# Performance work log

Hardware: AMD Instinct MI355X
Metric: run time of the kernel (lower is better)

The kernel has to match this reference:

```python
import jax, jax.numpy as jnp
import numpy as np

B, L, D = 2, 2048, 1024
H, DH = 16, 64
HIDDEN = 4096
DILATION, WINDOW, CAUSAL = 2, 512, True
EPS = 1e-5


def _ln(x, g, b):
    m = jnp.mean(x, axis=-1, keepdims=True)
    v = jnp.mean(jnp.square(x - m), axis=-1, keepdims=True)
    return (x - m) * jax.lax.rsqrt(v + EPS) * g + b


def setup_inputs() -> dict:
    key = jax.random.key(0)
    ks = jax.random.split(key, 8)
    s = 0.02
    return {
        "x": jax.random.normal(ks[0], (B, L, D), jnp.float32),
        "ln1_g": jnp.ones((D,), jnp.float32),
        "ln1_b": jnp.zeros((D,), jnp.float32),
        "w_qkv": jax.random.normal(ks[1], (3 * D, D), jnp.float32) * s,
        "b_qkv": jnp.zeros((3 * D,), jnp.float32),
        "w_o": jax.random.normal(ks[2], (D, D), jnp.float32) * s,
        "b_o": jnp.zeros((D,), jnp.float32),
        "ln2_g": jnp.ones((D,), jnp.float32),
        "ln2_b": jnp.zeros((D,), jnp.float32),
        "w_ff1": jax.random.normal(ks[3], (HIDDEN, D), jnp.float32) * s,
        "b_ff1": jnp.zeros((HIDDEN,), jnp.float32),
        "w_ff2": jax.random.normal(ks[4], (D, HIDDEN), jnp.float32) * s,
        "b_ff2": jnp.zeros((D,), jnp.float32),
    }


def reference(x, ln1_g, ln1_b, w_qkv, b_qkv, w_o, b_o, ln2_g, ln2_b, w_ff1, b_ff1, w_ff2, b_ff2):
    # pre-norm attention block with dilated/windowed/causal mask
    h = _ln(x, ln1_g, ln1_b)
    qkv = h @ w_qkv.T + b_qkv                      # [B, L, 3D]
    q, k, v = jnp.split(qkv, 3, axis=-1)
    q = q.reshape(B, L, H, DH)
    k = k.reshape(B, L, H, DH)
    v = v.reshape(B, L, H, DH)

    scale = 1.0 / jnp.sqrt(jnp.float32(DH))
    scores = jnp.einsum("bqhd,bkhd->bhqk", q, k) * scale  # [B, H, L, L]

    i = jnp.arange(L)[:, None]
    j = jnp.arange(L)[None, :]
    allowed = ((i - j) % DILATION == 0) & (jnp.abs(i - j) <= WINDOW)
    if CAUSAL:
        allowed = allowed & (j <= i)
    scores = jnp.where(allowed, scores, -jnp.inf)  # diagonal always allowed -> rows finite

    p = jax.nn.softmax(scores, axis=-1)
    attn = jnp.einsum("bhqk,bkhd->bqhd", p, v).reshape(B, L, D)

    out = x + attn @ w_o.T + b_o                   # residual 1 (dropout p=0)

    h2 = _ln(out, ln2_g, ln2_b)
    ff = jax.nn.gelu(h2 @ w_ff1.T + b_ff1, approximate=False) @ w_ff2.T + b_ff2
    return out + ff                                # residual 2
```

## Files before the change

kernel.cpp:

```cpp
#include <hip/hip_runtime.h>
#include <hip/hip_bf16.h>
#include <cmath>

#define Bsz 2
#define Lseq 2048
#define Dmod 1024
#define Hhead 16
#define DH 64
#define HID 4096
#define ROWS (Bsz * Lseq)
#define TD (3 * Dmod)

typedef __attribute__((ext_vector_type(8))) short bf16x8;
typedef __attribute__((ext_vector_type(4))) float f32x4;
typedef unsigned short ushort_t;

typedef const __attribute__((address_space(1))) void gv_t;
typedef __attribute__((address_space(3))) void lv_t;
#define GLDS16(GP, LP) __builtin_amdgcn_global_load_lds((gv_t*)(GP), (lv_t*)(LP), 16, 0, 0)

__device__ __forceinline__ float bf2f(short u)
{
    return __uint_as_float(((unsigned)(unsigned short)u) << 16);
}
__device__ __forceinline__ unsigned pack2(float a, float b)
{
    __hip_bfloat162 t;
    t.x = __float2bfloat16(a);
    t.y = __float2bfloat16(b);
    return *reinterpret_cast<unsigned*>(&t);
}
__device__ __forceinline__ float gelu_exact(float t)
{
    return 0.5f * t * (1.0f + erff(t * 0.70710678118654752f));
}

__device__ __forceinline__ void xcd_remap(int& mblk, int& nblk)
{
    int nx = gridDim.x;
    int nwg = nx * gridDim.y;
    int id = blockIdx.y * nx + blockIdx.x;
    int cpx = nwg >> 3;
    int swz = (id & 7) * cpx + (id >> 3);
    mblk = swz / nx;
    nblk = swz % nx;
}

__global__ __launch_bounds__(256) void f2b4_kernel(const float* __restrict__ s0, ushort_t* __restrict__ d0,
                                                   const float* __restrict__ s1, ushort_t* __restrict__ d1,
                                                   const float* __restrict__ s2, ushort_t* __restrict__ d2,
                                                   const float* __restrict__ s3, ushort_t* __restrict__ d3)
{
    int blk = blockIdx.x;
    const float* src;
    ushort_t* dst;
    int base;
    if (blk < 3072)      { src = s0; dst = d0; base = blk; }
    else if (blk < 4096) { src = s1; dst = d1; base = blk - 3072; }
    else if (blk < 8192) { src = s2; dst = d2; base = blk - 4096; }
    else                 { src = s3; dst = d3; base = blk - 8192; }
    int i = base * 256 + threadIdx.x;
    float4 v = reinterpret_cast<const float4*>(src)[i];
    uint2 o;
    o.x = pack2(v.x, v.y);
    o.y = pack2(v.z, v.w);
    reinterpret_cast<uint2*>(dst)[i] = o;
}

__global__ __launch_bounds__(256) void ln_kernel(const float* __restrict__ x,
                                                 const float* __restrict__ g,
                                                 const float* __restrict__ bta,
                                                 ushort_t* __restrict__ out)
{
    int row = blockIdx.x;
    int t = threadIdx.x;
    const float4* xr = reinterpret_cast<const float4*>(x) + (size_t)row * 256;
    float4 v = xr[t];
    float s  = v.x + v.y + v.z + v.w;
    float s2 = v.x * v.x + v.y * v.y + v.z * v.z + v.w * v.w;
#pragma unroll
    for (int o = 32; o > 0; o >>= 1) {
        s  += __shfl_down(s, o);
        s2 += __shfl_down(s2, o);
    }
    __shared__ float sa[4], sb[4];
    int wv = t >> 6, ln = t & 63;
    if (ln == 0) { sa[wv] = s; sb[wv] = s2; }
    __syncthreads();
    s  = sa[0] + sa[1] + sa[2] + sa[3];
    s2 = sb[0] + sb[1] + sb[2] + sb[3];
    float mean = s * (1.0f / 1024.0f);
    float var  = s2 * (1.0f / 1024.0f) - mean * mean;
    float inv  = rsqrtf(var + 1e-5f);
    float4 gv = reinterpret_cast<const float4*>(g)[t];
    float4 bv = reinterpret_cast<const float4*>(bta)[t];
    uint2 o;
    o.x = pack2((v.x - mean) * inv * gv.x + bv.x, (v.y - mean) * inv * gv.y + bv.y);
    o.y = pack2((v.z - mean) * inv * gv.z + bv.z, (v.w - mean) * inv * gv.w + bv.w);
    reinterpret_cast<uint2*>(out)[(size_t)row * 256 + t] = o;
}

__device__ __forceinline__ void gemm_n64_body(const ushort_t* __restrict__ A,
                                              const ushort_t* __restrict__ W,
                                              const float* __restrict__ bias,
                                              const float* __restrict__ res,
                                              void* __restrict__ C,
                                              int M, int N, int K, int ldw,
                                              int act, int obf)
{
    __shared__ ushort_t As0[128 * 64];
    __shared__ ushort_t Bs0[64 * 64];
    __shared__ ushort_t As1[128 * 64];
    __shared__ ushort_t Bs1[64 * 64];

    int tid = threadIdx.x;
    int w = tid >> 6, lane = tid & 63;
    int mblk, nblk;
    xcd_remap(mblk, nblk);
    int m0 = mblk * 128, n0 = nblk * 64;
    int wr = (w >> 1) * 64, wc = (w & 1) * 32;

    int srow = lane >> 3;
    int scol = (((lane & 7) ^ (lane >> 3)) & 7) * 8;
    const ushort_t* ga[4];
    const ushort_t* gb[2];
    int laofs[4], lbofs[2];
#pragma unroll
    for (int q = 0; q < 4; ++q) {
        ga[q] = A + (size_t)(m0 + w * 32 + q * 8 + srow) * K + scol;
        laofs[q] = (w * 32 + q * 8) * 64;
    }
#pragma unroll
    for (int q = 0; q < 2; ++q) {
        gb[q] = W + (size_t)(n0 + w * 16 + q * 8 + srow) * ldw + scol;
        lbofs[q] = (w * 16 + q * 8) * 64;
    }

    int fr = lane & 15;
    int fg = lane >> 4;
    int r0 = fg * 4;
    int cc = fr;

    f32x4 acc[4][2] = {};

    auto stage = [&](ushort_t* AS, ushort_t* BS, int k0) {
#pragma unroll
        for (int q = 0; q < 4; ++q) GLDS16(ga[q] + k0, AS + laofs[q]);
#pragma unroll
        for (int q = 0; q < 2; ++q) GLDS16(gb[q] + k0, BS + lbofs[q]);
    };
    auto compute = [&](const ushort_t* AS, const ushort_t* BS) {
#pragma unroll
        for (int kk = 0; kk < 2; ++kk) {
            bf16x8 af[4], bfr[2];
            int ca = ((kk * 4 + fg) ^ (fr & 7)) * 8;
#pragma unroll
            for (int i = 0; i < 4; ++i)
                af[i] = *reinterpret_cast<const bf16x8*>(&AS[(wr + i * 16 + fr) * 64 + ca]);
#pragma unroll
            for (int i = 0; i < 2; ++i)
                bfr[i] = *reinterpret_cast<const bf16x8*>(&BS[(wc + i * 16 + fr) * 64 + ca]);
#pragma unroll
            for (int mi = 0; mi < 4; ++mi)
#pragma unroll
                for (int ni = 0; ni < 2; ++ni)
                    acc[mi][ni] = __builtin_amdgcn_mfma_f32_16x16x32_bf16(
                        af[mi], bfr[ni], acc[mi][ni], 0, 0, 0);
        }
    };

    int nt = K >> 6;
    stage(As0, Bs0, 0);
    stage(As1, Bs1, 64);
    int t = 0;
    for (; t + 3 < nt; t += 2) {
        asm volatile("s_waitcnt vmcnt(6)" ::: "memory");
        __builtin_amdgcn_s_barrier();
        __builtin_amdgcn_sched_barrier(0);
        compute(As0, Bs0);
        __builtin_amdgcn_s_barrier();
        stage(As0, Bs0, (t + 2) * 64);

        asm volatile("s_waitcnt vmcnt(6)" ::: "memory");
        __builtin_amdgcn_s_barrier();
        __builtin_amdgcn_sched_barrier(0);
        compute(As1, Bs1);
        __builtin_amdgcn_s_barrier();
        stage(As1, Bs1, (t + 3) * 64);
    }
    asm volatile("s_waitcnt vmcnt(6)" ::: "memory");
    __builtin_amdgcn_s_barrier();
    __builtin_amdgcn_sched_barrier(0);
    compute(As0, Bs0);
    asm volatile("s_waitcnt vmcnt(0)" ::: "memory");
    __builtin_amdgcn_s_barrier();
    __builtin_amdgcn_sched_barrier(0);
    compute(As1, Bs1);

    float bv[2];
#pragma unroll
    for (int ni = 0; ni < 2; ++ni)
        bv[ni] = bias ? bias[n0 + wc + ni * 16 + cc] : 0.0f;

#pragma unroll
    for (int mi = 0; mi < 4; ++mi) {
#pragma unroll
        for (int r = 0; r < 4; ++r) {
            int row = m0 + wr + mi * 16 + r0 + r;
            const float* resrow = res ? res + (size_t)row * N : nullptr;
#pragma unroll
            for (int ni = 0; ni < 2; ++ni) {
                int col = n0 + wc + ni * 16 + cc;
                float v = acc[mi][ni][r] + bv[ni];
                if (act == 1) v = gelu_exact(v);
                if (resrow) v += resrow[col];
                if (obf) {
                    reinterpret_cast<ushort_t*>(C)[(size_t)row * N + col] =
                        (ushort_t)__bfloat16_as_ushort(__float2bfloat16(v));
                } else {
                    reinterpret_cast<float*>(C)[(size_t)row * N + col] = v;
                }
            }
        }
    }
}

__global__ __launch_bounds__(256) void gemm_a(const ushort_t* __restrict__ A,
                                              const ushort_t* __restrict__ W,
                                              const float* __restrict__ bias,
                                              const float* __restrict__ res,
                                              void* __restrict__ C,
                                              int M, int N, int K, int ldw,
                                              int act, int obf)
{
    gemm_n64_body(A, W, bias, res, C, M, N, K, ldw, act, obf);
}

__global__ __launch_bounds__(256) void gemm_b(const ushort_t* __restrict__ A,
                                              const ushort_t* __restrict__ W,
                                              const float* __restrict__ bias,
                                              const float* __restrict__ res,
                                              void* __restrict__ C,
                                              int M, int N, int K, int ldw,
                                              int act, int obf)
{
    gemm_n64_body(A, W, bias, res, C, M, N, K, ldw, act, obf);
}

__global__ __launch_bounds__(256) void attn_mfma(const ushort_t* __restrict__ qkv,
                                                 ushort_t* __restrict__ out)
{
    __shared__ ushort_t Vt[64][328];
    __shared__ ushort_t Pw[4][16][40];

    int bid = blockIdx.x;
    int qt = bid & 15, h = (bid >> 4) & 15, p = (bid >> 8) & 1, b = bid >> 9;
    int qt0 = qt * 64;
    int kstart = qt0 - 256;

    const ushort_t* base = qkv + (size_t)b * Lseq * TD;
    int tid = threadIdx.x;

#pragma unroll
    for (int it = 0; it < 10; ++it) {
        int idx = it * 256 + tid;
        int ko = idx >> 3;
        int dg = idx & 7;
        int kk = kstart + ko;
        bf16x8 v = {};
        if (kk >= 0)
            v = *reinterpret_cast<const bf16x8*>(base + (size_t)(2 * kk + p) * TD + 2048 + h * 64 + dg * 8);
        int kos = ko ^ (dg << 3);
#pragma unroll
        for (int j = 0; j < 8; ++j)
            Vt[dg * 8 + j][kos] = (ushort_t)v[j];
    }

    int w = tid >> 6, lane = tid & 63;
    int fr = lane & 15, fg = lane >> 4;
    int qw = qt0 + w * 16;
    const ushort_t* qrow = base + (size_t)(2 * (qw + fr) + p) * TD + h * 64;
    bf16x8 qf0 = *reinterpret_cast<const bf16x8*>(qrow + fg * 8);
    bf16x8 qf1 = *reinterpret_cast<const bf16x8*>(qrow + 32 + fg * 8);

    __syncthreads();

    float m[4]    = {-1e30f, -1e30f, -1e30f, -1e30f};
    float lsum[4] = {};
    f32x4 o[4]    = {};
    const float scale = 0.125f;
    int qbase = qw + fg * 4;

    for (int t = 0; t < 10; ++t) {
        int kt0 = kstart + t * 32;
        int kk0 = kt0 + fr, kk1 = kk0 + 16;
        int kk0c = kk0 < 0 ? 0 : kk0;
        int kk1c = kk1 < 0 ? 0 : kk1;
        const ushort_t* kr0 = base + (size_t)(2 * kk0c + p) * TD + 1024 + h * 64;
        const ushort_t* kr1 = base + (size_t)(2 * kk1c + p) * TD + 1024 + h * 64;
        bf16x8 k00 = *reinterpret_cast<const bf16x8*>(kr0 + fg * 8);
        bf16x8 k01 = *reinterpret_cast<const bf16x8*>(kr0 + 32 + fg * 8);
        bf16x8 k10 = *reinterpret_cast<const bf16x8*>(kr1 + fg * 8);
        bf16x8 k11 = *reinterpret_cast<const bf16x8*>(kr1 + 32 + fg * 8);

        f32x4 s0 = {}, s1 = {};
        s0 = __builtin_amdgcn_mfma_f32_16x16x32_bf16(qf0, k00, s0, 0, 0, 0);
        s0 = __builtin_amdgcn_mfma_f32_16x16x32_bf16(qf1, k01, s0, 0, 0, 0);
        s1 = __builtin_amdgcn_mfma_f32_16x16x32_bf16(qf0, k10, s1, 0, 0, 0);
        s1 = __builtin_amdgcn_mfma_f32_16x16x32_bf16(qf1, k11, s1, 0, 0, 0);

        int c0 = kt0 + fr, c1 = c0 + 16;
        float v0[4], v1[4], tmax[4];
#pragma unroll
        for (int r = 0; r < 4; ++r) {
            int qq = qbase + r;
            bool a0 = (c0 >= 0) && (c0 <= qq) && (c0 >= qq - 256);
            bool a1 = (c1 >= 0) && (c1 <= qq) && (c1 >= qq - 256);
            v0[r] = a0 ? s0[r] * scale : -1e30f;
            v1[r] = a1 ? s1[r] * scale : -1e30f;
            tmax[r] = fmaxf(v0[r], v1[r]);
        }
#pragma unroll
        for (int off = 1; off < 16; off <<= 1) {
#pragma unroll
            for (int r = 0; r < 4; ++r)
                tmax[r] = fmaxf(tmax[r], __shfl_xor(tmax[r], off));
        }
#pragma unroll
        for (int r = 0; r < 4; ++r) {
            float mn = fmaxf(m[r], tmax[r]);
            float corr = __expf(m[r] - mn);
            m[r] = mn;
            float p0 = __expf(v0[r] - mn);
            float p1 = __expf(v1[r] - mn);
            lsum[r] = lsum[r] * corr + p0 + p1;
#pragma unroll
            for (int db = 0; db < 4; ++db)
                o[db][r] *= corr;
            Pw[w][fg * 4 + r][fr]      = (ushort_t)__bfloat16_as_ushort(__float2bfloat16(p0));
            Pw[w][fg * 4 + r][fr + 16] = (ushort_t)__bfloat16_as_ushort(__float2bfloat16(p1));
        }

        bf16x8 pf = *reinterpret_cast<const bf16x8*>(&Pw[w][fr][fg * 8]);
#pragma unroll
        for (int db = 0; db < 4; ++db) {
            int row = db * 16 + fr;
            int colc = (t * 32 + fg * 8) ^ ((row >> 3) << 3);
            bf16x8 vf = *reinterpret_cast<const bf16x8*>(&Vt[row][colc]);
            o[db] = __builtin_amdgcn_mfma_f32_16x16x32_bf16(pf, vf, o[db], 0, 0, 0);
        }
    }

#pragma unroll
    for (int off = 1; off < 16; off <<= 1) {
#pragma unroll
        for (int r = 0; r < 4; ++r)
            lsum[r] += __shfl_xor(lsum[r], off);
    }
    float inv[4];
#pragma unroll
    for (int r = 0; r < 4; ++r) inv[r] = 1.0f / lsum[r];

#pragma unroll
    for (int r = 0; r < 4; ++r) {
        size_t orow = ((size_t)b * Lseq + 2 * (qbase + r) + p) * Dmod + h * 64;
#pragma unroll
        for (int db = 0; db < 4; ++db)
            out[orow + db * 16 + fr] =
                (ushort_t)__bfloat16_as_ushort(__float2bfloat16(o[db][r] * inv[r]));
    }
}

extern "C" void kernel_launch(void* const* d_in, const int* in_sizes, int n_in,
                              void* d_out, int out_size, void* d_ws, size_t ws_size,
                              hipStream_t stream)
{
    const float* x     = (const float*)d_in[0];
    const float* ln1_g = (const float*)d_in[1];
    const float* ln1_b = (const float*)d_in[2];
    const float* w_qkv = (const float*)d_in[3];
    const float* b_qkv = (const float*)d_in[4];
    const float* w_o   = (const float*)d_in[5];
    const float* b_o   = (const float*)d_in[6];
    const float* ln2_g = (const float*)d_in[7];
    const float* ln2_b = (const float*)d_in[8];
    const float* w_ff1 = (const float*)d_in[9];
    const float* b_ff1 = (const float*)d_in[10];
    const float* w_ff2 = (const float*)d_in[11];
    const float* b_ff2 = (const float*)d_in[12];
    float* out = (float*)d_out;

    ushort_t* wq     = (ushort_t*)d_ws;
    ushort_t* wo     = wq  + (size_t)TD * Dmod;
    ushort_t* wf1    = wo  + (size_t)Dmod * Dmod;
    ushort_t* wf2    = wf1 + (size_t)HID * Dmod;
    ushort_t* bufFF  = wf2 + (size_t)Dmod * HID;
    ushort_t* bufH   = bufFF + (size_t)ROWS * HID;
    ushort_t* bufAtt = bufH + (size_t)ROWS * Dmod;

    f2b4_kernel<<<12288, 256, 0, stream>>>(w_qkv, wq, w_o, wo, w_ff1, wf1, w_ff2, wf2);

    ln_kernel<<<ROWS, 256, 0, stream>>>(x, ln1_g, ln1_b, bufH);
    gemm_a<<<dim3(TD / 64, ROWS / 128), 256, 0, stream>>>(bufH, wq, b_qkv, nullptr,
                                                          bufFF, ROWS, TD, Dmod, Dmod, 0, 1);
    attn_mfma<<<Bsz * 2 * Hhead * (1024 / 64), 256, 0, stream>>>(bufFF, bufAtt);
    gemm_b<<<dim3(Dmod / 64, ROWS / 128), 256, 0, stream>>>(bufAtt, wo, b_o, x,
                                                            out, ROWS, Dmod, Dmod, Dmod, 0, 0);
    ln_kernel<<<ROWS, 256, 0, stream>>>(out, ln2_g, ln2_b, bufH);
    gemm_a<<<dim3(HID / 64, ROWS / 128), 256, 0, stream>>>(bufH, wf1, b_ff1, nullptr,
                                                           bufFF, ROWS, HID, Dmod, Dmod, 1, 1);
    gemm_b<<<dim3(Dmod / 64, ROWS / 128), 256, 0, stream>>>(bufFF, wf2, b_ff2, out,
                                                            out, ROWS, Dmod, HID, HID, 0, 0);
}
```

Measured before the change: 230.3 us.

## Fuse fp32-to-bf16 weight conversion into GEMM B-tile staging

Removes the separate weight-conversion kernel. The GEMMs now load fp32 weight tiles into registers, convert them to bf16 and write them swizzled into LDS, instead of using direct global-to-LDS loads of pre-converted bf16 weights. This saves one launch and the write and re-read of the bf16 weight copy. The cost is that every M-block re-reads fp32 weights, twice the bytes, and does the conversion again. It also adds VGPR pressure and an LDS-write wait inside the pipelined main loop.

Result: slower. 308.5 us (+34.0%).

```diff
diff --git a/kernel.cpp b/kernel.cpp
--- a/kernel.cpp
+++ b/kernel.cpp
@@ -44,27 +44,6 @@
     int swz = (id & 7) * cpx + (id >> 3);
     mblk = swz / nx;
     nblk = swz % nx;
-}
-
-__global__ __launch_bounds__(256) void f2b4_kernel(const float* __restrict__ s0, ushort_t* __restrict__ d0,
-                                                   const float* __restrict__ s1, ushort_t* __restrict__ d1,
-                                                   const float* __restrict__ s2, ushort_t* __restrict__ d2,
-                                                   const float* __restrict__ s3, ushort_t* __restrict__ d3)
-{
-    int blk = blockIdx.x;
-    const float* src;
-    ushort_t* dst;
-    int base;
-    if (blk < 3072)      { src = s0; dst = d0; base = blk; }
-    else if (blk < 4096) { src = s1; dst = d1; base = blk - 3072; }
-    else if (blk < 8192) { src = s2; dst = d2; base = blk - 4096; }
-    else                 { src = s3; dst = d3; base = blk - 8192; }
-    int i = base * 256 + threadIdx.x;
-    float4 v = reinterpret_cast<const float4*>(src)[i];
-    uint2 o;
-    o.x = pack2(v.x, v.y);
-    o.y = pack2(v.z, v.w);
-    reinterpret_cast<uint2*>(dst)[i] = o;
 }
 
 __global__ __launch_bounds__(256) void ln_kernel(const float* __restrict__ x,
@@ -100,8 +79,13 @@
     reinterpret_cast<uint2*>(out)[(size_t)row * 256 + t] = o;
 }
 
+struct BReg {
+    float4 a, b;
+    float4 c, d;
+};
+
 __device__ __forceinline__ void gemm_n64_body(const ushort_t* __restrict__ A,
-                                              const ushort_t* __restrict__ W,
+                                              const float* __restrict__ Wf,
                                               const float* __restrict__ bias,
                                               const float* __restrict__ res,
                                               void* __restrict__ C,
@@ -121,19 +105,21 @@
     int wr = (w >> 1) * 64, wc = (w & 1) * 32;
 
     int srow = lane >> 3;
-    int scol = (((lane & 7) ^ (lane >> 3)) & 7) * 8;
+    int csrc = ((lane & 7) ^ srow) & 7;
+    int scol = csrc * 8;
     const ushort_t* ga[4];
-    const ushort_t* gb[2];
-    int laofs[4], lbofs[2];
+    int laofs[4];
 #pragma unroll
     for (int q = 0; q < 4; ++q) {
         ga[q] = A + (size_t)(m0 + w * 32 + q * 8 + srow) * K + scol;
         laofs[q] = (w * 32 + q * 8) * 64;
     }
+    const float* gbF[2];
+    int bwofs[2];
 #pragma unroll
     for (int q = 0; q < 2; ++q) {
-        gb[q] = W + (size_t)(n0 + w * 16 + q * 8 + srow) * ldw + scol;
-        lbofs[q] = (w * 16 + q * 8) * 64;
+        gbF[q] = Wf + (size_t)(n0 + w * 16 + q * 8 + srow) * ldw + scol;
+        bwofs[q] = (w * 16 + q * 8 + srow) * 64 + (lane & 7) * 8;
     }
 
     int fr = lane & 15;
@@ -143,11 +129,24 @@
 
     f32x4 acc[4][2] = {};
 
-    auto stage = [&](ushort_t* AS, ushort_t* BS, int k0) {
+    auto stageA = [&](ushort_t* AS, int k0) {
 #pragma unroll
         for (int q = 0; q < 4; ++q) GLDS16(ga[q] + k0, AS + laofs[q]);
-#pragma unroll
-        for (int q = 0; q < 2; ++q) GLDS16(gb[q] + k0, BS + lbofs[q]);
+    };
+    auto loadB = [&](BReg& R, int k0) {
+        R.a = *reinterpret_cast<const float4*>(gbF[0] + k0);
+        R.b = *reinterpret_cast<const float4*>(gbF[0] + k0 + 4);
+        R.c = *reinterpret_cast<const float4*>(gbF[1] + k0);
+        R.d = *reinterpret_cast<const float4*>(gbF[1] + k0 + 4);
+    };
+    auto cvtwrite = [&](ushort_t* BS, const BReg& R) {
+        uint4 u0, u1;
+        u0.x = pack2(R.a.x, R.a.y); u0.y = pack2(R.a.z, R.a.w);
+        u0.z = pack2(R.b.x, R.b.y); u0.w = pack2(R.b.z, R.b.w);
+        u1.x = pack2(R.c.x, R.c.y); u1.y = pack2(R.c.z, R.c.w);
+        u1.z = pack2(R.d.x, R.d.y); u1.w = pack2(R.d.z, R.d.w);
+        *reinterpret_cast<uint4*>(&BS[bwofs[0]]) = u0;
+        *reinterpret_cast<uint4*>(&BS[bwofs[1]]) = u1;
     };
     auto compute = [&](const ushort_t* AS, const ushort_t* BS) {
 #pragma unroll
@@ -170,29 +169,41 @@
     };
 
     int nt = K >> 6;
-    stage(As0, Bs0, 0);
-    stage(As1, Bs1, 64);
+    BReg Br0, Br1;
+    stageA(As0, 0);   loadB(Br0, 0);
+    stageA(As1, 64);  loadB(Br1, 64);
     int t = 0;
     for (; t + 3 < nt; t += 2) {
-        asm volatile("s_waitcnt vmcnt(6)" ::: "memory");
+        asm volatile("s_waitcnt vmcnt(8)" ::: "memory");
+        cvtwrite(Bs0, Br0);
+        asm volatile("s_waitcnt lgkmcnt(0)" ::: "memory");
         __builtin_amdgcn_s_barrier();
         __builtin_amdgcn_sched_barrier(0);
         compute(As0, Bs0);
         __builtin_amdgcn_s_barrier();
-        stage(As0, Bs0, (t + 2) * 64);
-
-        asm volatile("s_waitcnt vmcnt(6)" ::: "memory");
+        stageA(As0, (t + 2) * 64);
+        loadB(Br0, (t + 2) * 64);
+
+        asm volatile("s_waitcnt vmcnt(8)" ::: "memory");
+        cvtwrite(Bs1, Br1);
+        asm volatile("s_waitcnt lgkmcnt(0)" ::: "memory");
         __builtin_amdgcn_s_barrier();
         __builtin_amdgcn_sched_barrier(0);
         compute(As1, Bs1);
         __builtin_amdgcn_s_barrier();
-        stage(As1, Bs1, (t + 3) * 64);
-    }
-    asm volatile("s_waitcnt vmcnt(6)" ::: "memory");
+        stageA(As1, (t + 3) * 64);
+        loadB(Br1, (t + 3) * 64);
+    }
+    asm volatile("s_waitcnt vmcnt(8)" ::: "memory");
+    cvtwrite(Bs0, Br0);
+    asm volatile("s_waitcnt lgkmcnt(0)" ::: "memory");
     __builtin_amdgcn_s_barrier();
     __builtin_amdgcn_sched_barrier(0);
     compute(As0, Bs0);
+    __builtin_amdgcn_s_barrier();
     asm volatile("s_waitcnt vmcnt(0)" ::: "memory");
+    cvtwrite(Bs1, Br1);
+    asm volatile("s_waitcnt lgkmcnt(0)" ::: "memory");
     __builtin_amdgcn_s_barrier();
     __builtin_amdgcn_sched_barrier(0);
     compute(As1, Bs1);
@@ -226,25 +237,25 @@
 }
 
 __global__ __launch_bounds__(256) void gemm_a(const ushort_t* __restrict__ A,
-                                              const ushort_t* __restrict__ W,
+                                              const float* __restrict__ Wf,
                                               const float* __restrict__ bias,
                                               const float* __restrict__ res,
                                               void* __restrict__ C,
                                               int M, int N, int K, int ldw,
                                               int act, int obf)
 {
-    gemm_n64_body(A, W, bias, res, C, M, N, K, ldw, act, obf);
+    gemm_n64_body(A, Wf, bias, res, C, M, N, K, ldw, act, obf);
 }
 
 __global__ __launch_bounds__(256) void gemm_b(const ushort_t* __restrict__ A,
-                                              const ushort_t* __restrict__ W,
+                                              const float* __restrict__ Wf,
                                               const float* __restrict__ bias,
                                               const float* __restrict__ res,
                                               void* __restrict__ C,
                                               int M, int N, int K, int ldw,
                                               int act, int obf)
 {
-    gemm_n64_body(A, W, bias, res, C, M, N, K, ldw, act, obf);
+    gemm_n64_body(A, Wf, bias, res, C, M, N, K, ldw, act, obf);
 }
 
 __global__ __launch_bounds__(256) void attn_mfma(const ushort_t* __restrict__ qkv,
@@ -390,25 +401,19 @@
     const float* b_ff2 = (const float*)d_in[12];
     float* out = (float*)d_out;
 
-    ushort_t* wq     = (ushort_t*)d_ws;
-    ushort_t* wo     = wq  + (size_t)TD * Dmod;
-    ushort_t* wf1    = wo  + (size_t)Dmod * Dmod;
-    ushort_t* wf2    = wf1 + (size_t)HID * Dmod;
-    ushort_t* bufFF  = wf2 + (size_t)Dmod * HID;
+    ushort_t* bufFF  = (ushort_t*)d_ws;
     ushort_t* bufH   = bufFF + (size_t)ROWS * HID;
     ushort_t* bufAtt = bufH + (size_t)ROWS * Dmod;
 
-    f2b4_kernel<<<12288, 256, 0, stream>>>(w_qkv, wq, w_o, wo, w_ff1, wf1, w_ff2, wf2);
-
     ln_kernel<<<ROWS, 256, 0, stream>>>(x, ln1_g, ln1_b, bufH);
-    gemm_a<<<dim3(TD / 64, ROWS / 128), 256, 0, stream>>>(bufH, wq, b_qkv, nullptr,
+    gemm_a<<<dim3(TD / 64, ROWS / 128), 256, 0, stream>>>(bufH, w_qkv, b_qkv, nullptr,
                                                           bufFF, ROWS, TD, Dmod, Dmod, 0, 1);
     attn_mfma<<<Bsz * 2 * Hhead * (1024 / 64), 256, 0, stream>>>(bufFF, bufAtt);
-    gemm_b<<<dim3(Dmod / 64, ROWS / 128), 256, 0, stream>>>(bufAtt, wo, b_o, x,
+    gemm_b<<<dim3(Dmod / 64, ROWS / 128), 256, 0, stream>>>(bufAtt, w_o, b_o, x,
                                                             out, ROWS, Dmod, Dmod, Dmod, 0, 0);
     ln_kernel<<<ROWS, 256, 0, stream>>>(out, ln2_g, ln2_b, bufH);
-    gemm_a<<<dim3(HID / 64, ROWS / 128), 256, 0, stream>>>(bufH, wf1, b_ff1, nullptr,
+    gemm_a<<<dim3(HID / 64, ROWS / 128), 256, 0, stream>>>(bufH, w_ff1, b_ff1, nullptr,
                                                            bufFF, ROWS, HID, Dmod, Dmod, 1, 1);
-    gemm_b<<<dim3(Dmod / 64, ROWS / 128), 256, 0, stream>>>(bufFF, wf2, b_ff2, out,
+    gemm_b<<<dim3(Dmod / 64, ROWS / 128), 256, 0, stream>>>(bufFF, w_ff2, b_ff2, out,
                                                             out, ROWS, Dmod, HID, HID, 0, 0);
 }
```
